# Kernel tuning notes

Hardware: AMD Instinct MI355X
Metric: run time of the kernel (lower is better)

## Reference

```python
import jax, jax.numpy as jnp
import numpy as np

N_NODES = 100000
HIDDEN = 64
IN_CH = 61


def setup_inputs() -> dict:
    key = jax.random.key(0)
    ks = jax.random.split(key, 12)
    x = jax.random.normal(ks[0], (N_NODES, IN_CH), dtype=jnp.float32)
    edge_index = jax.random.randint(ks[1], (2, 3200000), 0, N_NODES, dtype=jnp.int64)
    s = 0.1
    # GCNConv weights (lin: in->hidden, bias separate)
    W1 = jax.random.normal(ks[2], (IN_CH, HIDDEN), dtype=jnp.float32) * s
    b1 = jnp.zeros((HIDDEN,), dtype=jnp.float32)
    W2 = jax.random.normal(ks[3], (HIDDEN, HIDDEN), dtype=jnp.float32) * s
    b2 = jnp.zeros((HIDDEN,), dtype=jnp.float32)
    W3 = jax.random.normal(ks[4], (HIDDEN, HIDDEN), dtype=jnp.float32) * s
    b3 = jnp.zeros((HIDDEN,), dtype=jnp.float32)
    # MLP head: Linear(64,64) -> ReLU -> Linear(64,1)
    Wh1 = jax.random.normal(ks[5], (HIDDEN, HIDDEN), dtype=jnp.float32) * s
    bh1 = jnp.zeros((HIDDEN,), dtype=jnp.float32)
    Wh2 = jax.random.normal(ks[6], (HIDDEN, 1), dtype=jnp.float32) * s
    bh2 = jnp.zeros((1,), dtype=jnp.float32)
    return {"x": x, "edge_index": edge_index,
            "W1": W1, "b1": b1, "W2": W2, "b2": b2, "W3": W3, "b3": b3,
            "Wh1": Wh1, "bh1": bh1, "Wh2": Wh2, "bh2": bh2}


def _gcn_layer(x, W, b, src, dst, norm, n):
    # x' = scatter_add_{dst}( norm_e * (xW)[src] ) + b   (self-loops already in src/dst)
    h = x @ W                                    # (N, out)
    msg = norm[:, None] * h[src]                 # (E', out) gather
    agg = jax.ops.segment_sum(msg, dst, num_segments=n)  # scatter-add
    return agg + b


def reference(x, edge_index, W1, b1, W2, b2, W3, b3, Wh1, bh1, Wh2, bh2):
    n = x.shape[0]
    # add self-loops (GCNConv default add_self_loops=True)
    loop = jnp.arange(n, dtype=edge_index.dtype)
    src = jnp.concatenate([edge_index[0], loop])
    dst = jnp.concatenate([edge_index[1], loop])
    # symmetric normalization: deg from in-degree (dst), norm = d^-1/2[src]*d^-1/2[dst]
    deg = jax.ops.segment_sum(jnp.ones_like(dst, dtype=x.dtype), dst, num_segments=n)
    dinv = jnp.where(deg > 0, jax.lax.rsqrt(deg), 0.0)
    norm = dinv[src] * dinv[dst]
    h = x
    for (W, b) in ((W1, b1), (W2, b2), (W3, b3)):
        h = jax.nn.relu(_gcn_layer(h, W, b, src, dst, norm, n))
        # dropout: identity in eval mode
    # MLP head
    h = jax.nn.relu(h @ Wh1 + bh1)
    out = (h @ Wh2 + bh2).squeeze(-1)            # (N,)
    return out
```

## Files before the change

### kernel.cpp

```cpp
#include <hip/hip_runtime.h>
#include <hip/hip_fp16.h>

#define HID 64
#define FSH 8
#define FB 392
#define SCAP 9216
#define FCH 4096

__global__ void zero_kernel(int* __restrict__ p, int n) {
    int i = blockIdx.x * blockDim.x + threadIdx.x;
    if (i < n) p[i] = 0;
}

__global__ __launch_bounds__(256) void fillA_kernel(const int* __restrict__ src,
                                                    const int* __restrict__ dst,
                                                    int* __restrict__ gcur,
                                                    unsigned int* __restrict__ recA,
                                                    int E) {
    __shared__ unsigned int srec[FCH];
    __shared__ int hist[FB], lbase[FB], lcur[FB], gpos[FB];
    __shared__ int buf[256];
    int t = threadIdx.x;
    int base = blockIdx.x * FCH;
    int lim = E - base;
    if (lim > FCH) lim = FCH;
    if (lim <= 0) return;
    for (int i = t; i < FB; i += 256) hist[i] = 0;
    __syncthreads();
    for (int i = t; i < lim; i += 256) atomicAdd(&hist[dst[base + i] >> FSH], 1);
    __syncthreads();
    int i0 = 2 * t, i1 = 2 * t + 1;
    int a0 = (i0 < FB) ? hist[i0] : 0;
    int a1 = (i1 < FB) ? hist[i1] : 0;
    int pair = a0 + a1;
    buf[t] = pair;
    __syncthreads();
#pragma unroll
    for (int o = 1; o < 256; o <<= 1) {
        int v = (t >= o) ? buf[t - o] : 0;
        __syncthreads();
        buf[t] += v;
        __syncthreads();
    }
    int excl = buf[t] - pair;
    if (i0 < FB) { lbase[i0] = excl;      lcur[i0] = excl; }
    if (i1 < FB) { lbase[i1] = excl + a0; lcur[i1] = excl + a0; }
    __syncthreads();
    for (int i = t; i < FB; i += 256) gpos[i] = atomicAdd(&gcur[i], hist[i]);
    __syncthreads();
    for (int i = t; i < lim; i += 256) {
        int d = dst[base + i];
        int s = src[base + i];
        int bkt = d >> FSH;
        int idx = atomicAdd(&lcur[bkt], 1);
        srec[idx] = ((unsigned int)(d & ((1 << FSH) - 1)) << 17) | (unsigned int)s;
    }
    __syncthreads();
    int g16 = t >> 4, lane = t & 15;
    for (int bkt = g16; bkt < FB; bkt += 16) {
        int L = hist[bkt], lb = lbase[bkt], gp = gpos[bkt];
        for (int j = lane; j < L; j += 16) {
            int g = gp + j;
            if (g < SCAP) recA[(size_t)bkt * SCAP + g] = srec[lb + j];
        }
    }
}

__global__ __launch_bounds__(256) void bucketscan_kernel(const int* __restrict__ gcur,
                                                         int* __restrict__ bbase) {
    __shared__ int buf[256];
    int t = threadIdx.x;
    int i0 = 2 * t, i1 = 2 * t + 1;
    int a0 = (i0 < FB) ? min(gcur[i0], SCAP) : 0;
    int a1 = (i1 < FB) ? min(gcur[i1], SCAP) : 0;
    int pair = a0 + a1;
    buf[t] = pair;
    __syncthreads();
#pragma unroll
    for (int o = 1; o < 256; o <<= 1) {
        int v = (t >= o) ? buf[t - o] : 0;
        __syncthreads();
        buf[t] += v;
        __syncthreads();
    }
    int excl = buf[t] - pair;
    if (i0 < FB) bbase[i0] = excl;
    if (i1 < FB) bbase[i1] = excl + a0;
}

__global__ __launch_bounds__(256) void fillB_kernel(const int* __restrict__ gcur,
                                                    const int* __restrict__ bbase,
                                                    const unsigned int* __restrict__ recA,
                                                    int* __restrict__ rowptr,
                                                    float* __restrict__ dinv,
                                                    int* __restrict__ col, int N) {
    __shared__ unsigned int lcol[SCAP];
    __shared__ int hist[256], cur[256], buf[256];
    int b = blockIdx.x, t = threadIdx.x;
    int n0 = b << FSH;
    hist[t] = 0;
    __syncthreads();
    int cnt = gcur[b];
    if (cnt > SCAP) cnt = SCAP;
    const unsigned int* rA = recA + (size_t)b * SCAP;
    for (int r = t; r < cnt; r += 256) atomicAdd(&hist[rA[r] >> 17], 1);
    __syncthreads();
    int a = hist[t];
    buf[t] = a;
    __syncthreads();
#pragma unroll
    for (int o = 1; o < 256; o <<= 1) {
        int v = (t >= o) ? buf[t - o] : 0;
        __syncthreads();
        buf[t] += v;
        __syncthreads();
    }
    int excl = buf[t] - a;
    int node = n0 + t;
    int rbase = bbase[b];
    if (node <= N) rowptr[node] = rbase + excl;
    if (node < N) dinv[node] = 1.0f / sqrtf((float)(a + 1));
    cur[t] = excl;
    __syncthreads();
    for (int r = t; r < cnt; r += 256) {
        unsigned int rec = rA[r];
        int pos = atomicAdd(&cur[rec >> 17], 1);
        lcol[pos] = rec & 0x1ffffu;
    }
    __syncthreads();
    for (int j = t; j < cnt; j += 256) col[rbase + j] = (int)lcol[j];
}

template <int K, typename XT>
__global__ __launch_bounds__(256) void linscale_kernel(const XT* __restrict__ x,
                                                       const float* __restrict__ W,
                                                       const float* __restrict__ dinv,
                                                       __half* __restrict__ out, int N) {
    __shared__ float4 Wl[K * 16];
    const float4* W4 = reinterpret_cast<const float4*>(W);
    for (int i = threadIdx.x; i < K * 16; i += blockDim.x) Wl[i] = W4[i];
    __syncthreads();
    int node = blockIdx.x * blockDim.x + threadIdx.x;
    if (node >= N) return;
    float4 acc[16];
#pragma unroll
    for (int c = 0; c < 16; ++c) acc[c] = make_float4(0.f, 0.f, 0.f, 0.f);
    const XT* xr = x + (size_t)node * K;
    for (int k = 0; k < K; ++k) {
        float xv = (float)xr[k];
#pragma unroll
        for (int c = 0; c < 16; ++c) {
            float4 w = Wl[k * 16 + c];
            acc[c].x += xv * w.x;
            acc[c].y += xv * w.y;
            acc[c].z += xv * w.z;
            acc[c].w += xv * w.w;
        }
    }
    float dv = dinv[node];
    __half2* o = reinterpret_cast<__half2*>(out + (size_t)node * HID);
#pragma unroll
    for (int c = 0; c < 16; ++c) {
        o[c * 2 + 0] = __floats2half2_rn(acc[c].x * dv, acc[c].y * dv);
        o[c * 2 + 1] = __floats2half2_rn(acc[c].z * dv, acc[c].w * dv);
    }
}

__global__ __launch_bounds__(256) void gather_kernel(const int* __restrict__ rowptr,
                                                     const int* __restrict__ col,
                                                     const float* __restrict__ dinv,
                                                     const __half2* __restrict__ hs2,
                                                     const float* __restrict__ b,
                                                     __half2* __restrict__ out2, int N) {
    int lane = threadIdx.x & 63;
    int hf = lane >> 5;
    int gl = lane & 31;
    int wid = (blockIdx.x * blockDim.x + threadIdx.x) >> 6;
    int nw = (gridDim.x * blockDim.x) >> 6;
    float bx = b[2 * gl], by = b[2 * gl + 1];
    for (int dbase = wid * 2; dbase < N; dbase += nw * 2) {
        int d = dbase + hf;
        bool act = d < N;
        int dd = act ? d : N - 1;
        int beg = rowptr[dd];
        int end = act ? rowptr[dd + 1] : beg;
        float2 acc = __half22float2(hs2[((size_t)dd << 5) + gl]);
        for (int ebase = beg; ebase < end; ebase += 32) {
            int e = ebase + gl;
            int cv = (e < end) ? col[e] : 0;
            int cnt = end - ebase;
            if (cnt > 32) cnt = 32;
            int k = 0;
            for (; k + 4 <= cnt; k += 4) {
                int s0 = __shfl(cv, k + 0, 32);
                int s1 = __shfl(cv, k + 1, 32);
                int s2 = __shfl(cv, k + 2, 32);
                int s3 = __shfl(cv, k + 3, 32);
                float2 v0 = __half22float2(hs2[((size_t)s0 << 5) + gl]);
                float2 v1 = __half22float2(hs2[((size_t)s1 << 5) + gl]);
                float2 v2 = __half22float2(hs2[((size_t)s2 << 5) + gl]);
                float2 v3 = __half22float2(hs2[((size_t)s3 << 5) + gl]);
                acc.x += (v0.x + v1.x) + (v2.x + v3.x);
                acc.y += (v0.y + v1.y) + (v2.y + v3.y);
            }
            for (; k < cnt; ++k) {
                int s = __shfl(cv, k, 32);
                float2 v = __half22float2(hs2[((size_t)s << 5) + gl]);
                acc.x += v.x; acc.y += v.y;
            }
        }
        if (act) {
            float dv = dinv[d];
            float rx = fmaxf(fmaf(acc.x, dv, bx), 0.f);
            float ry = fmaxf(fmaf(acc.y, dv, by), 0.f);
            out2[((size_t)d << 5) + gl] = __floats2half2_rn(rx, ry);
        }
    }
}

__global__ __launch_bounds__(256) void head_kernel(const __half* __restrict__ h,
                                                   const float* __restrict__ Wh1,
                                                   const float* __restrict__ bh1,
                                                   const float* __restrict__ Wh2,
                                                   const float* __restrict__ bh2,
                                                   float* __restrict__ out, int N) {
    __shared__ float4 Wl[64 * 16];
    __shared__ float bhs[64];
    __shared__ float w2s[64];
    const float4* W4 = reinterpret_cast<const float4*>(Wh1);
    for (int i = threadIdx.x; i < 64 * 16; i += blockDim.x) Wl[i] = W4[i];
    if (threadIdx.x < 64) {
        bhs[threadIdx.x] = bh1[threadIdx.x];
        w2s[threadIdx.x] = Wh2[threadIdx.x];
    }
    __syncthreads();
    int node = blockIdx.x * blockDim.x + threadIdx.x;
    if (node >= N) return;
    float4 acc[16];
#pragma unroll
    for (int c = 0; c < 16; ++c) acc[c] = make_float4(0.f, 0.f, 0.f, 0.f);
    const __half* hr = h + ((size_t)node << 6);
    for (int k = 0; k < 64; ++k) {
        float xv = __half2float(hr[k]);
#pragma unroll
        for (int c = 0; c < 16; ++c) {
            float4 w = Wl[k * 16 + c];
            acc[c].x += xv * w.x;
            acc[c].y += xv * w.y;
            acc[c].z += xv * w.z;
            acc[c].w += xv * w.w;
        }
    }
    float o = 0.f;
#pragma unroll
    for (int c = 0; c < 16; ++c) {
        o += fmaxf(acc[c].x + bhs[4 * c + 0], 0.f) * w2s[4 * c + 0];
        o += fmaxf(acc[c].y + bhs[4 * c + 1], 0.f) * w2s[4 * c + 1];
        o += fmaxf(acc[c].z + bhs[4 * c + 2], 0.f) * w2s[4 * c + 2];
        o += fmaxf(acc[c].w + bhs[4 * c + 3], 0.f) * w2s[4 * c + 3];
    }
    out[node] = o + bh2[0];
}

extern "C" void kernel_launch(void* const* d_in, const int* in_sizes, int n_in,
                              void* d_out, int out_size, void* d_ws, size_t ws_size,
                              hipStream_t stream) {
    const float* x = (const float*)d_in[0];
    const int* edge = (const int*)d_in[1];
    const float* W1 = (const float*)d_in[2];
    const float* b1 = (const float*)d_in[3];
    const float* W2 = (const float*)d_in[4];
    const float* b2 = (const float*)d_in[5];
    const float* W3 = (const float*)d_in[6];
    const float* b3 = (const float*)d_in[7];
    const float* Wh1 = (const float*)d_in[8];
    const float* bh1 = (const float*)d_in[9];
    const float* Wh2 = (const float*)d_in[10];
    const float* bh2 = (const float*)d_in[11];

    int N = in_sizes[0] / 61;
    int E = in_sizes[1] / 2;
    const int* srcs = edge;
    const int* dsts = edge + E;
    float* out = (float*)d_out;

    char* ws = (char*)d_ws;
    size_t off = 0;
    auto alloc = [&](size_t bytes) {
        void* p = ws + off;
        off += (bytes + 255) & ~(size_t)255;
        return p;
    };
    float* dinv = (float*)alloc((size_t)N * 4);
    int* rowptr = (int*)alloc((size_t)(N + 1) * 4);
    int* gcur = (int*)alloc((size_t)FB * 4);
    int* bbase = (int*)alloc((size_t)FB * 4);
    int* col = (int*)alloc((size_t)E * 4);
    __half* Ah = (__half*)alloc((size_t)N * HID * 2);
    __half* Bh = (__half*)alloc((size_t)N * HID * 2);
    if (off > ws_size) return;
    unsigned int* recA = (unsigned int*)Ah;

    int gN = (N + 255) / 256;
    int gA = (E + FCH - 1) / FCH;

    zero_kernel<<<(FB + 255) / 256, 256, 0, stream>>>(gcur, FB);
    fillA_kernel<<<gA, 256, 0, stream>>>(srcs, dsts, gcur, recA, E);
    bucketscan_kernel<<<1, 256, 0, stream>>>(gcur, bbase);
    fillB_kernel<<<FB, 256, 0, stream>>>(gcur, bbase, recA, rowptr, dinv, col, N);

    linscale_kernel<61, float><<<gN, 256, 0, stream>>>(x, W1, dinv, Bh, N);
    gather_kernel<<<4096, 256, 0, stream>>>(rowptr, col, dinv,
                                            (const __half2*)Bh, b1, (__half2*)Ah, N);

    linscale_kernel<64, __half><<<gN, 256, 0, stream>>>(Ah, W2, dinv, Bh, N);
    gather_kernel<<<4096, 256, 0, stream>>>(rowptr, col, dinv,
                                            (const __half2*)Bh, b2, (__half2*)Ah, N);

    linscale_kernel<64, __half><<<gN, 256, 0, stream>>>(Ah, W3, dinv, Bh, N);
    gather_kernel<<<4096, 256, 0, stream>>>(rowptr, col, dinv,
                                            (const __half2*)Bh, b3, (__half2*)Ah, N);

    head_kernel<<<gN, 256, 0, stream>>>(Ah, Wh1, bh1, Wh2, bh2, out, N);
}
```

Measured before the change: 414.8 us.

## Batch gather loads, vectorize half row reads, fold bucket scan into fillB

Removes the single-block bucketscan launch. Each fillB block now computes its own base offset by reducing the preceding bucket counts. The gather kernel issues 16 independent row loads per batch, masking tail lanes instead of branching, and keeps two accumulators, aiming to raise memory-level parallelism on the random gathers. The half-precision linear and head kernels now read each 64-wide row as eight 16-byte vector loads instead of scalar half loads. The risks are extra wasted loads on short rows, since lanes past the row end still load row 0, and more register pressure.

```diff
diff --git a/kernel.cpp b/kernel.cpp
--- a/kernel.cpp
+++ b/kernel.cpp
@@ -6,6 +6,11 @@
 #define FB 392
 #define SCAP 9216
 #define FCH 4096
+
+__device__ __forceinline__ float2 h2f2(unsigned int bits) {
+    __half2 h = __builtin_bit_cast(__half2, bits);
+    return __half22float2(h);
+}
 
 __global__ void zero_kernel(int* __restrict__ p, int n) {
     int i = blockIdx.x * blockDim.x + threadIdx.x;
@@ -66,30 +71,7 @@
     }
 }
 
-__global__ __launch_bounds__(256) void bucketscan_kernel(const int* __restrict__ gcur,
-                                                         int* __restrict__ bbase) {
-    __shared__ int buf[256];
-    int t = threadIdx.x;
-    int i0 = 2 * t, i1 = 2 * t + 1;
-    int a0 = (i0 < FB) ? min(gcur[i0], SCAP) : 0;
-    int a1 = (i1 < FB) ? min(gcur[i1], SCAP) : 0;
-    int pair = a0 + a1;
-    buf[t] = pair;
-    __syncthreads();
-#pragma unroll
-    for (int o = 1; o < 256; o <<= 1) {
-        int v = (t >= o) ? buf[t - o] : 0;
-        __syncthreads();
-        buf[t] += v;
-        __syncthreads();
-    }
-    int excl = buf[t] - pair;
-    if (i0 < FB) bbase[i0] = excl;
-    if (i1 < FB) bbase[i1] = excl + a0;
-}
-
 __global__ __launch_bounds__(256) void fillB_kernel(const int* __restrict__ gcur,
-                                                    const int* __restrict__ bbase,
                                                     const unsigned int* __restrict__ recA,
                                                     int* __restrict__ rowptr,
                                                     float* __restrict__ dinv,
@@ -98,6 +80,17 @@
     __shared__ int hist[256], cur[256], buf[256];
     int b = blockIdx.x, t = threadIdx.x;
     int n0 = b << FSH;
+    int p = 0;
+    for (int i = t; i < b; i += 256) p += min(gcur[i], SCAP);
+    buf[t] = p;
+    __syncthreads();
+#pragma unroll
+    for (int o = 128; o > 0; o >>= 1) {
+        if (t < o) buf[t] += buf[t + o];
+        __syncthreads();
+    }
+    int rbase = buf[0];
+    __syncthreads();
     hist[t] = 0;
     __syncthreads();
     int cnt = gcur[b];
@@ -117,7 +110,6 @@
     }
     int excl = buf[t] - a;
     int node = n0 + t;
-    int rbase = bbase[b];
     if (node <= N) rowptr[node] = rbase + excl;
     if (node < N) dinv[node] = 1.0f / sqrtf((float)(a + 1));
     cur[t] = excl;
@@ -131,23 +123,22 @@
     for (int j = t; j < cnt; j += 256) col[rbase + j] = (int)lcol[j];
 }
 
-template <int K, typename XT>
-__global__ __launch_bounds__(256) void linscale_kernel(const XT* __restrict__ x,
-                                                       const float* __restrict__ W,
-                                                       const float* __restrict__ dinv,
-                                                       __half* __restrict__ out, int N) {
-    __shared__ float4 Wl[K * 16];
+__global__ __launch_bounds__(256) void linscale61_kernel(const float* __restrict__ x,
+                                                         const float* __restrict__ W,
+                                                         const float* __restrict__ dinv,
+                                                         __half* __restrict__ out, int N) {
+    __shared__ float4 Wl[61 * 16];
     const float4* W4 = reinterpret_cast<const float4*>(W);
-    for (int i = threadIdx.x; i < K * 16; i += blockDim.x) Wl[i] = W4[i];
+    for (int i = threadIdx.x; i < 61 * 16; i += blockDim.x) Wl[i] = W4[i];
     __syncthreads();
     int node = blockIdx.x * blockDim.x + threadIdx.x;
     if (node >= N) return;
     float4 acc[16];
 #pragma unroll
     for (int c = 0; c < 16; ++c) acc[c] = make_float4(0.f, 0.f, 0.f, 0.f);
-    const XT* xr = x + (size_t)node * K;
-    for (int k = 0; k < K; ++k) {
-        float xv = (float)xr[k];
+    const float* xr = x + (size_t)node * 61;
+    for (int k = 0; k < 61; ++k) {
+        float xv = xr[k];
 #pragma unroll
         for (int c = 0; c < 16; ++c) {
             float4 w = Wl[k * 16 + c];
@@ -159,6 +150,47 @@
     }
     float dv = dinv[node];
     __half2* o = reinterpret_cast<__half2*>(out + (size_t)node * HID);
+#pragma unroll
+    for (int c = 0; c < 16; ++c) {
+        o[c * 2 + 0] = __floats2half2_rn(acc[c].x * dv, acc[c].y * dv);
+        o[c * 2 + 1] = __floats2half2_rn(acc[c].z * dv, acc[c].w * dv);
+    }
+}
+
+__global__ __launch_bounds__(256) void linscale64h_kernel(const __half* __restrict__ x,
+                                                          const float* __restrict__ W,
+                                                          const float* __restrict__ dinv,
+                                                          __half* __restrict__ out, int N) {
+    __shared__ float4 Wl[64 * 16];
+    const float4* W4 = reinterpret_cast<const float4*>(W);
+    for (int i = threadIdx.x; i < 64 * 16; i += blockDim.x) Wl[i] = W4[i];
+    __syncthreads();
+    int node = blockIdx.x * blockDim.x + threadIdx.x;
+    if (node >= N) return;
+    float4 acc[16];
+#pragma unroll
+    for (int c = 0; c < 16; ++c) acc[c] = make_float4(0.f, 0.f, 0.f, 0.f);
+    const uint4* xr4 = reinterpret_cast<const uint4*>(x + ((size_t)node << 6));
+#pragma unroll
+    for (int c8 = 0; c8 < 8; ++c8) {
+        uint4 pk = xr4[c8];
+        float2 f0 = h2f2(pk.x), f1 = h2f2(pk.y), f2 = h2f2(pk.z), f3 = h2f2(pk.w);
+        float xv[8] = {f0.x, f0.y, f1.x, f1.y, f2.x, f2.y, f3.x, f3.y};
+#pragma unroll
+        for (int j = 0; j < 8; ++j) {
+            int k = c8 * 8 + j;
+#pragma unroll
+            for (int c = 0; c < 16; ++c) {
+                float4 w = Wl[k * 16 + c];
+                acc[c].x += xv[j] * w.x;
+                acc[c].y += xv[j] * w.y;
+                acc[c].z += xv[j] * w.z;
+                acc[c].w += xv[j] * w.w;
+            }
+        }
+    }
+    float dv = dinv[node];
+    __half2* o = reinterpret_cast<__half2*>(out + ((size_t)node << 6));
 #pragma unroll
     for (int c = 0; c < 16; ++c) {
         o[c * 2 + 0] = __floats2half2_rn(acc[c].x * dv, acc[c].y * dv);
@@ -184,35 +216,47 @@
         int dd = act ? d : N - 1;
         int beg = rowptr[dd];
         int end = act ? rowptr[dd + 1] : beg;
-        float2 acc = __half22float2(hs2[((size_t)dd << 5) + gl]);
+        float2 acc0 = __half22float2(hs2[((size_t)dd << 5) + gl]);
+        float2 acc1 = make_float2(0.f, 0.f);
         for (int ebase = beg; ebase < end; ebase += 32) {
             int e = ebase + gl;
             int cv = (e < end) ? col[e] : 0;
             int cnt = end - ebase;
-            if (cnt > 32) cnt = 32;
-            int k = 0;
-            for (; k + 4 <= cnt; k += 4) {
-                int s0 = __shfl(cv, k + 0, 32);
-                int s1 = __shfl(cv, k + 1, 32);
-                int s2 = __shfl(cv, k + 2, 32);
-                int s3 = __shfl(cv, k + 3, 32);
-                float2 v0 = __half22float2(hs2[((size_t)s0 << 5) + gl]);
-                float2 v1 = __half22float2(hs2[((size_t)s1 << 5) + gl]);
-                float2 v2 = __half22float2(hs2[((size_t)s2 << 5) + gl]);
-                float2 v3 = __half22float2(hs2[((size_t)s3 << 5) + gl]);
-                acc.x += (v0.x + v1.x) + (v2.x + v3.x);
-                acc.y += (v0.y + v1.y) + (v2.y + v3.y);
+            {
+                unsigned int r[16];
+#pragma unroll
+                for (int k = 0; k < 16; ++k) {
+                    int s = __shfl(cv, k, 32);
+                    r[k] = *reinterpret_cast<const unsigned int*>(hs2 + ((size_t)s << 5) + gl);
+                }
+#pragma unroll
+                for (int k = 0; k < 16; ++k) {
+                    unsigned int bits = (k < cnt) ? r[k] : 0u;
+                    float2 v = h2f2(bits);
+                    if (k & 1) { acc1.x += v.x; acc1.y += v.y; }
+                    else       { acc0.x += v.x; acc0.y += v.y; }
+                }
             }
-            for (; k < cnt; ++k) {
-                int s = __shfl(cv, k, 32);
-                float2 v = __half22float2(hs2[((size_t)s << 5) + gl]);
-                acc.x += v.x; acc.y += v.y;
+            if (cnt > 16) {
+                unsigned int r[16];
+#pragma unroll
+                for (int k = 0; k < 16; ++k) {
+                    int s = __shfl(cv, k + 16, 32);
+                    r[k] = *reinterpret_cast<const unsigned int*>(hs2 + ((size_t)s << 5) + gl);
+                }
+#pragma unroll
+                for (int k = 0; k < 16; ++k) {
+                    unsigned int bits = (k + 16 < cnt) ? r[k] : 0u;
+                    float2 v = h2f2(bits);
+                    if (k & 1) { acc1.x += v.x; acc1.y += v.y; }
+                    else       { acc0.x += v.x; acc0.y += v.y; }
+                }
             }
         }
         if (act) {
             float dv = dinv[d];
-            float rx = fmaxf(fmaf(acc.x, dv, bx), 0.f);
-            float ry = fmaxf(fmaf(acc.y, dv, by), 0.f);
+            float rx = fmaxf(fmaf(acc0.x + acc1.x, dv, bx), 0.f);
+            float ry = fmaxf(fmaf(acc0.y + acc1.y, dv, by), 0.f);
             out2[((size_t)d << 5) + gl] = __floats2half2_rn(rx, ry);
         }
     }
@@ -239,16 +283,23 @@
     float4 acc[16];
 #pragma unroll
     for (int c = 0; c < 16; ++c) acc[c] = make_float4(0.f, 0.f, 0.f, 0.f);
-    const __half* hr = h + ((size_t)node << 6);
-    for (int k = 0; k < 64; ++k) {
-        float xv = __half2float(hr[k]);
-#pragma unroll
-        for (int c = 0; c < 16; ++c) {
-            float4 w = Wl[k * 16 + c];
-            acc[c].x += xv * w.x;
-            acc[c].y += xv * w.y;
-            acc[c].z += xv * w.z;
-            acc[c].w += xv * w.w;
+    const uint4* hr4 = reinterpret_cast<const uint4*>(h + ((size_t)node << 6));
+#pragma unroll
+    for (int c8 = 0; c8 < 8; ++c8) {
+        uint4 pk = hr4[c8];
+        float2 f0 = h2f2(pk.x), f1 = h2f2(pk.y), f2 = h2f2(pk.z), f3 = h2f2(pk.w);
+        float xv[8] = {f0.x, f0.y, f1.x, f1.y, f2.x, f2.y, f3.x, f3.y};
+#pragma unroll
+        for (int j = 0; j < 8; ++j) {
+            int k = c8 * 8 + j;
+#pragma unroll
+            for (int c = 0; c < 16; ++c) {
+                float4 w = Wl[k * 16 + c];
+                acc[c].x += xv[j] * w.x;
+                acc[c].y += xv[j] * w.y;
+                acc[c].z += xv[j] * w.z;
+                acc[c].w += xv[j] * w.w;
+            }
         }
     }
     float o = 0.f;
@@ -294,7 +345,6 @@
     float* dinv = (float*)alloc((size_t)N * 4);
     int* rowptr = (int*)alloc((size_t)(N + 1) * 4);
     int* gcur = (int*)alloc((size_t)FB * 4);
-    int* bbase = (int*)alloc((size_t)FB * 4);
     int* col = (int*)alloc((size_t)E * 4);
     __half* Ah = (__half*)alloc((size_t)N * HID * 2);
     __half* Bh = (__half*)alloc((size_t)N * HID * 2);
@@ -306,18 +356,17 @@
 
     zero_kernel<<<(FB + 255) / 256, 256, 0, stream>>>(gcur, FB);
     fillA_kernel<<<gA, 256, 0, stream>>>(srcs, dsts, gcur, recA, E);
-    bucketscan_kernel<<<1, 256, 0, stream>>>(gcur, bbase);
-    fillB_kernel<<<FB, 256, 0, stream>>>(gcur, bbase, recA, rowptr, dinv, col, N);
-
-    linscale_kernel<61, float><<<gN, 256, 0, stream>>>(x, W1, dinv, Bh, N);
+    fillB_kernel<<<FB, 256, 0, stream>>>(gcur, recA, rowptr, dinv, col, N);
+
+    linscale61_kernel<<<gN, 256, 0, stream>>>(x, W1, dinv, Bh, N);
     gather_kernel<<<4096, 256, 0, stream>>>(rowptr, col, dinv,
                                             (const __half2*)Bh, b1, (__half2*)Ah, N);
 
-    linscale_kernel<64, __half><<<gN, 256, 0, stream>>>(Ah, W2, dinv, Bh, N);
+    linscale64h_kernel<<<gN, 256, 0, stream>>>(Ah, W2, dinv, Bh, N);
     gather_kernel<<<4096, 256, 0, stream>>>(rowptr, col, dinv,
                                             (const __half2*)Bh, b2, (__half2*)Ah, N);
 
-    linscale_kernel<64, __half><<<gN, 256, 0, stream>>>(Ah, W3, dinv, Bh, N);
+    linscale64h_kernel<<<gN, 256, 0, stream>>>(Ah, W3, dinv, Bh, N);
     gather_kernel<<<4096, 256, 0, stream>>>(rowptr, col, dinv,
                                             (const __half2*)Bh, b3, (__half2*)Ah, N);
 
```

Result: faster. 351.7 us (-15.2%).
